# Optimization experiments

Measured on AMD Instinct MI355X. Metric: run time of the kernel, lower is better.

## Reference

```python
import jax, jax.numpy as jnp
import numpy as np

NUM_LAYERS = 3
CODEBOOK_SIZE = 2048
EMBED_DIM = 256
B, T = 16, 2048


def setup_inputs() -> dict:
    key = jax.random.key(0)
    k1, k2 = jax.random.split(key)
    h = jax.random.normal(k1, (B, T, EMBED_DIM), dtype=jnp.float32)
    codebooks = jax.random.normal(k2, (NUM_LAYERS, CODEBOOK_SIZE, EMBED_DIM), dtype=jnp.float32)
    return {"h": h, "codebooks": codebooks}


def reference(h, codebooks):
    """Residual VQ: 3 sequential layers of nearest-codeword quantization.
    h: (B, T, D); codebooks: (L, K, D).
    Returns (quantized_total (B,T,D), indices (L, B, T)).
    """
    residual = h
    quantized_total = jnp.zeros_like(h)
    all_indices = []
    for l in range(codebooks.shape[0]):
        W = codebooks[l]  # (K, D)
        # ||r - w||^2 = ||r||^2 - 2 r.w + ||w||^2 ; same argmin as the naive broadcast form.
        r_sq = jnp.sum(residual * residual, axis=-1, keepdims=True)         # (B, T, 1)
        w_sq = jnp.sum(W * W, axis=-1)                                      # (K,)
        cross = jnp.einsum('btd,kd->btk', residual, W)                      # (B, T, K)
        dists = r_sq - 2.0 * cross + w_sq                                   # (B, T, K)
        indices = jnp.argmin(dists, axis=-1)                                # (B, T)
        all_indices.append(indices)
        quant = W[indices]                                                  # gather -> (B, T, D)
        quantized_total = quantized_total + quant
        residual = residual - quant
    return quantized_total, jnp.stack(all_indices, axis=0)
```

## Files before the change

kernel.cpp:

```cpp
#include <hip/hip_runtime.h>
#include <math.h>

#define NUM_LAYERS 3
#define KCB 2048
#define DIM 256
#define NROWS 32768
#define NQ (NROWS * DIM)

#define F_BYTES (3u * 128u * 16384u)

#define BSH_OFF  0
#define XCH_OFF  65536
#define RSQP_OFF 98304
#define BV_OFF   99328
#define BI_OFF   100352
#define BIDX_OFF 101376
#define SMEM_BYTES 101888

typedef _Float16 half8 __attribute__((ext_vector_type(8)));
typedef float   f32x4 __attribute__((ext_vector_type(4)));

__global__ void rvq_wsq(const float* __restrict__ cb, float* __restrict__ wsq)
{
    int tid = blockIdx.x * 256 + threadIdx.x;
    const float* p = cb + (size_t)tid * DIM;
    float s = 0.f;
    #pragma unroll
    for (int u = 0; u < 64; ++u) {
        float4 v = *(const float4*)(p + u * 4);
        s = fmaf(v.x, v.x, s); s = fmaf(v.y, v.y, s);
        s = fmaf(v.z, v.z, s); s = fmaf(v.w, v.w, s);
    }
    wsq[tid] = s;
}

__global__ void rvq_repack(const float* __restrict__ cb, unsigned short* __restrict__ F)
{
    int b = blockIdx.x;
    int layer = b >> 10;
    int rem   = b & 1023;
    int tn    = rem >> 3;
    int kb    = rem & 7;
    int lane  = threadIdx.x;

    int cw = tn * 16 + (lane & 15);
    int k0 = kb * 32 + (lane >> 4) * 8;
    const float* src = cb + ((size_t)(layer * KCB + cw)) * DIM + k0;
    float4 x0 = *(const float4*)(src);
    float4 x1 = *(const float4*)(src + 4);
    float v[8] = {x0.x, x0.y, x0.z, x0.w, x1.x, x1.y, x1.z, x1.w};

    half8 hi, lo;
    #pragma unroll
    for (int j = 0; j < 8; ++j) {
        _Float16 h = (_Float16)v[j];
        hi[j] = h;
        lo[j] = (_Float16)(v[j] - (float)h);
    }
    size_t base = ((size_t)b) * 1024;
    *(half8*)(F + base + lane * 8)        = hi;
    *(half8*)(F + base + 512 + lane * 8)  = lo;
}

__device__ __forceinline__ void stage_chunk32(const char* Fb, char* dst, int c, int t)
{
    const char* g = Fb + (size_t)c * 32768;
    #pragma unroll
    for (int i = 0; i < 4; ++i) {
        int off = (i * 512 + t) * 16;
        __builtin_amdgcn_global_load_lds(
            (const __attribute__((address_space(1))) unsigned int*)(g + off),
            (__attribute__((address_space(3))) unsigned int*)(dst + off), 16, 0, 0);
    }
}

__device__ __forceinline__ void tile_partial(
    const char* tbase, const half8 (&ahi)[2][4], const half8 (&alo)[2][4],
    int kt, int lane, f32x4 (&po)[2])
{
    const f32x4 z = {0.f, 0.f, 0.f, 0.f};
    f32x4 a00 = z, a01 = z, a10 = z, a11 = z;
    #pragma unroll
    for (int kq = 0; kq < 4; ++kq) {
        const int kb = kt * 4 + kq;
        half8 bhi = *(const half8*)(tbase + kb * 2048 + lane * 16);
        half8 blo = *(const half8*)(tbase + kb * 2048 + 1024 + lane * 16);
        if (kq & 1) {
            a01 = __builtin_amdgcn_mfma_f32_16x16x32_f16(ahi[0][kq], bhi, a01, 0, 0, 0);
            a11 = __builtin_amdgcn_mfma_f32_16x16x32_f16(ahi[1][kq], bhi, a11, 0, 0, 0);
            a01 = __builtin_amdgcn_mfma_f32_16x16x32_f16(alo[0][kq], bhi, a01, 0, 0, 0);
            a11 = __builtin_amdgcn_mfma_f32_16x16x32_f16(alo[1][kq], bhi, a11, 0, 0, 0);
            a01 = __builtin_amdgcn_mfma_f32_16x16x32_f16(ahi[0][kq], blo, a01, 0, 0, 0);
            a11 = __builtin_amdgcn_mfma_f32_16x16x32_f16(ahi[1][kq], blo, a11, 0, 0, 0);
        } else {
            a00 = __builtin_amdgcn_mfma_f32_16x16x32_f16(ahi[0][kq], bhi, a00, 0, 0, 0);
            a10 = __builtin_amdgcn_mfma_f32_16x16x32_f16(ahi[1][kq], bhi, a10, 0, 0, 0);
            a00 = __builtin_amdgcn_mfma_f32_16x16x32_f16(alo[0][kq], bhi, a00, 0, 0, 0);
            a10 = __builtin_amdgcn_mfma_f32_16x16x32_f16(alo[1][kq], bhi, a10, 0, 0, 0);
            a00 = __builtin_amdgcn_mfma_f32_16x16x32_f16(ahi[0][kq], blo, a00, 0, 0, 0);
            a10 = __builtin_amdgcn_mfma_f32_16x16x32_f16(ahi[1][kq], blo, a10, 0, 0, 0);
        }
    }
    #pragma unroll
    for (int i = 0; i < 4; ++i) { po[0][i] = a00[i] + a01[i]; po[1][i] = a10[i] + a11[i]; }
}

__global__ __launch_bounds__(512, 2)
void rvq_main(const float* __restrict__ h,
              const float* __restrict__ cb,
              const unsigned short* __restrict__ F,
              const float* __restrict__ wsq,
              float* __restrict__ out)
{
    extern __shared__ char smem[];
    char*  Bsh     = smem + BSH_OFF;
    char*  Xch     = smem + XCH_OFF;
    float* rsqp    = (float*)(smem + RSQP_OFF);
    float* bV_sh   = (float*)(smem + BV_OFF);
    int*   bI_sh   = (int*)  (smem + BI_OFF);
    int*   bidx_sh = (int*)  (smem + BIDX_OFF);

    const int t     = threadIdx.x;
    const int lane  = t & 63;
    const int wv    = t >> 6;
    const int kt    = wv & 1;
    const int rg    = wv >> 1;
    const int rowB  = blockIdx.x * 128;
    const int row0w = rowB + rg * 32;
    const int arow  = lane & 15;
    const int aq    = lane >> 4;

    half8 ahi[2][4], alo[2][4];
    float s2[2];
    #pragma unroll
    for (int mi = 0; mi < 2; ++mi) {
        s2[mi] = 0.f;
        #pragma unroll
        for (int kq = 0; kq < 4; ++kq) {
            const float* p = h + (size_t)(row0w + mi * 16 + arow) * DIM + (kt * 4 + kq) * 32 + aq * 8;
            float4 x0 = *(const float4*)(p);
            float4 x1 = *(const float4*)(p + 4);
            float v[8] = {x0.x, x0.y, x0.z, x0.w, x1.x, x1.y, x1.z, x1.w};
            #pragma unroll
            for (int j = 0; j < 8; ++j) {
                _Float16 hv = (_Float16)v[j];
                ahi[mi][kq][j] = hv;
                alo[mi][kq][j] = (_Float16)(v[j] - (float)hv);
                s2[mi] = fmaf(v[j], v[j], s2[mi]);
            }
        }
    }

    stage_chunk32((const char*)F, Bsh, 0, t);

    for (int l = 0; l < NUM_LAYERS; ++l) {
        const float* __restrict__ Wl  = cb + (size_t)l * KCB * DIM;
        const float* __restrict__ wql = wsq + l * KCB;
        const char*  Fb = (const char*)F + (size_t)l * 2097152;

        float a0 = s2[0], a1 = s2[1];
        a0 += __shfl_xor(a0, 16); a0 += __shfl_xor(a0, 32);
        a1 += __shfl_xor(a1, 16); a1 += __shfl_xor(a1, 32);
        if (aq == 0) {
            rsqp[kt * 128 + rg * 32 + arow]      = a0;
            rsqp[kt * 128 + rg * 32 + 16 + arow] = a1;
        }
        __syncthreads();

        float rsqC[2][4];
        #pragma unroll
        for (int mi = 0; mi < 2; ++mi)
            #pragma unroll
            for (int i = 0; i < 4; ++i) {
                int row = rg * 32 + mi * 16 + aq * 4 + i;
                rsqC[mi][i] = rsqp[row] + rsqp[128 + row];
            }

        float bestV[2][4];
        int   bestI[2][4];
        #pragma unroll
        for (int mi = 0; mi < 2; ++mi)
            #pragma unroll
            for (int i = 0; i < 4; ++i) { bestV[mi][i] = INFINITY; bestI[mi][i] = 0; }

        for (int c = 0; c < 64; ++c) {
            const int cur = c & 1;
            if (c + 1 < 64) stage_chunk32(Fb, Bsh + (size_t)(1 - cur) * 32768, c + 1, t);
            const char* bb = Bsh + (size_t)cur * 32768;

            {
                f32x4 pn[2];
                tile_partial(bb + (size_t)(1 - kt) * 16384, ahi, alo, kt, lane, pn);
                char* xw = Xch + (size_t)cur * 16384 + rg * 4096 + kt * 2048;
                *(f32x4*)(xw + lane * 16)        = pn[0];
                *(f32x4*)(xw + 1024 + lane * 16) = pn[1];
            }
            f32x4 po[2];
            tile_partial(bb + (size_t)kt * 16384, ahi, alo, kt, lane, po);

            __syncthreads();

            const char* xr = Xch + (size_t)cur * 16384 + rg * 4096 + (1 - kt) * 2048;
            f32x4 pp0 = *(const f32x4*)(xr + lane * 16);
            f32x4 pp1 = *(const f32x4*)(xr + 1024 + lane * 16);

            const int col = c * 32 + kt * 16 + arow;
            const float wq = wql[col];
            #pragma unroll
            for (int i = 0; i < 4; ++i) {
                float c0 = po[0][i] + pp0[i];
                float d0 = (rsqC[0][i] - 2.f * c0) + wq;
                if (d0 < bestV[0][i]) { bestV[0][i] = d0; bestI[0][i] = col; }
                float c1 = po[1][i] + pp1[i];
                float d1 = (rsqC[1][i] - 2.f * c1) + wq;
                if (d1 < bestV[1][i]) { bestV[1][i] = d1; bestI[1][i] = col; }
            }
        }

        #pragma unroll
        for (int mi = 0; mi < 2; ++mi)
            #pragma unroll
            for (int i = 0; i < 4; ++i) {
                float bv = bestV[mi][i]; int bi = bestI[mi][i];
                #pragma unroll
                for (int s = 8; s; s >>= 1) {
                    float ov = __shfl_xor(bv, s, 16);
                    int   oi = __shfl_xor(bi, s, 16);
                    if (ov < bv || (ov == bv && oi < bi)) { bv = ov; bi = oi; }
                }
                bestV[mi][i] = bv; bestI[mi][i] = bi;
            }
        if (arow == 0) {
            #pragma unroll
            for (int mi = 0; mi < 2; ++mi)
                #pragma unroll
                for (int i = 0; i < 4; ++i) {
                    bV_sh[wv * 32 + mi * 16 + aq * 4 + i] = bestV[mi][i];
                    bI_sh[wv * 32 + mi * 16 + aq * 4 + i] = bestI[mi][i];
                }
        }
        __syncthreads();

        if (t < 128) {
            int rgi = t >> 5, rl = t & 31;
            float v0 = bV_sh[(rgi * 2 + 0) * 32 + rl]; int i0 = bI_sh[(rgi * 2 + 0) * 32 + rl];
            float v1 = bV_sh[(rgi * 2 + 1) * 32 + rl]; int i1 = bI_sh[(rgi * 2 + 1) * 32 + rl];
            int bi = (v1 < v0 || (v1 == v0 && i1 < i0)) ? i1 : i0;
            bidx_sh[t] = bi;
            out[NQ + (size_t)l * NROWS + rowB + t] = (float)bi;
        }
        if (l < NUM_LAYERS - 1)
            stage_chunk32(Fb + 2097152, Bsh, 0, t);
        __syncthreads();

        if (l < NUM_LAYERS - 1) {
            #pragma unroll
            for (int mi = 0; mi < 2; ++mi) {
                const int bi = bidx_sh[rg * 32 + mi * 16 + arow];
                const float* wrow = Wl + (size_t)bi * DIM;
                float ns = 0.f;
                #pragma unroll
                for (int kq = 0; kq < 4; ++kq) {
                    const float* wp = wrow + (kt * 4 + kq) * 32 + aq * 8;
                    float4 w0 = *(const float4*)(wp);
                    float4 w1 = *(const float4*)(wp + 4);
                    float wv8[8] = {w0.x, w0.y, w0.z, w0.w, w1.x, w1.y, w1.z, w1.w};
                    #pragma unroll
                    for (int j = 0; j < 8; ++j) {
                        float r = ((float)ahi[mi][kq][j] + (float)alo[mi][kq][j]) - wv8[j];
                        _Float16 hv = (_Float16)r;
                        ahi[mi][kq][j] = hv;
                        alo[mi][kq][j] = (_Float16)(r - (float)hv);
                        ns = fmaf(r, r, ns);
                    }
                }
                s2[mi] = ns;
            }
        } else {
            #pragma unroll
            for (int mi = 0; mi < 2; ++mi) {
                const int row = row0w + mi * 16 + arow;
                const int bi  = bidx_sh[rg * 32 + mi * 16 + arow];
                const float* wrow = Wl + (size_t)bi * DIM;
                #pragma unroll
                for (int kq = 0; kq < 4; ++kq) {
                    const int ko = (kt * 4 + kq) * 32 + aq * 8;
                    const float* wp = wrow + ko;
                    const float* hp = h + (size_t)row * DIM + ko;
                    float4 w0 = *(const float4*)(wp);
                    float4 w1 = *(const float4*)(wp + 4);
                    float4 h0 = *(const float4*)(hp);
                    float4 h1 = *(const float4*)(hp + 4);
                    float wv8[8] = {w0.x, w0.y, w0.z, w0.w, w1.x, w1.y, w1.z, w1.w};
                    float hv8[8] = {h0.x, h0.y, h0.z, h0.w, h1.x, h1.y, h1.z, h1.w};
                    float o[8];
                    #pragma unroll
                    for (int j = 0; j < 8; ++j) {
                        float r = ((float)ahi[mi][kq][j] + (float)alo[mi][kq][j]) - wv8[j];
                        o[j] = hv8[j] - r;
                    }
                    float* op = out + (size_t)row * DIM + ko;
                    *(float4*)(op)     = make_float4(o[0], o[1], o[2], o[3]);
                    *(float4*)(op + 4) = make_float4(o[4], o[5], o[6], o[7]);
                }
            }
        }
    }
}

extern "C" void kernel_launch(void* const* d_in, const int* in_sizes, int n_in,
                              void* d_out, int out_size, void* d_ws, size_t ws_size,
                              hipStream_t stream) {
    const float* h  = (const float*)d_in[0];
    const float* cb = (const float*)d_in[1];
    float* out = (float*)d_out;
    unsigned short* F = (unsigned short*)d_ws;
    float* wsq = (float*)((char*)d_ws + F_BYTES);

    hipFuncSetAttribute((const void*)rvq_main,
                        hipFuncAttributeMaxDynamicSharedMemorySize, SMEM_BYTES);

    rvq_wsq   <<<dim3(24),   dim3(256), 0, stream>>>(cb, wsq);
    rvq_repack<<<dim3(3072), dim3(64),  0, stream>>>(cb, F);
    rvq_main  <<<dim3(NROWS / 128), dim3(512), SMEM_BYTES, stream>>>(h, cb, F, wsq, out);
}
```

Baseline: 382.7 us.

## Give each wave full-K residual fragments and drop cross-wave partial-sum exchange

```diff
diff --git a/kernel.cpp b/kernel.cpp
--- a/kernel.cpp
+++ b/kernel.cpp
@@ -10,12 +10,11 @@
 #define F_BYTES (3u * 128u * 16384u)
 
 #define BSH_OFF  0
-#define XCH_OFF  65536
-#define RSQP_OFF 98304
-#define BV_OFF   99328
-#define BI_OFF   100352
-#define BIDX_OFF 101376
-#define SMEM_BYTES 101888
+#define BV_OFF   65536
+#define BI_OFF   66048
+#define BIDX_OFF 66560
+#define RSQ_OFF  66816
+#define SMEM_BYTES 67072
 
 typedef _Float16 half8 __attribute__((ext_vector_type(8)));
 typedef float   f32x4 __attribute__((ext_vector_type(4)));
@@ -66,46 +65,52 @@
 {
     const char* g = Fb + (size_t)c * 32768;
     #pragma unroll
-    for (int i = 0; i < 4; ++i) {
-        int off = (i * 512 + t) * 16;
+    for (int i = 0; i < 8; ++i) {
+        int off = (i * 256 + t) * 16;
         __builtin_amdgcn_global_load_lds(
             (const __attribute__((address_space(1))) unsigned int*)(g + off),
             (__attribute__((address_space(3))) unsigned int*)(dst + off), 16, 0, 0);
     }
 }
 
-__device__ __forceinline__ void tile_partial(
-    const char* tbase, const half8 (&ahi)[2][4], const half8 (&alo)[2][4],
-    int kt, int lane, f32x4 (&po)[2])
+__device__ __forceinline__ void tile_full(
+    const char* tbase, const half8 (&ahi)[2][8], const half8 (&alo)[2][8],
+    int lane, f32x4 (&po)[2])
 {
     const f32x4 z = {0.f, 0.f, 0.f, 0.f};
     f32x4 a00 = z, a01 = z, a10 = z, a11 = z;
-    #pragma unroll
-    for (int kq = 0; kq < 4; ++kq) {
-        const int kb = kt * 4 + kq;
-        half8 bhi = *(const half8*)(tbase + kb * 2048 + lane * 16);
-        half8 blo = *(const half8*)(tbase + kb * 2048 + 1024 + lane * 16);
-        if (kq & 1) {
-            a01 = __builtin_amdgcn_mfma_f32_16x16x32_f16(ahi[0][kq], bhi, a01, 0, 0, 0);
-            a11 = __builtin_amdgcn_mfma_f32_16x16x32_f16(ahi[1][kq], bhi, a11, 0, 0, 0);
-            a01 = __builtin_amdgcn_mfma_f32_16x16x32_f16(alo[0][kq], bhi, a01, 0, 0, 0);
-            a11 = __builtin_amdgcn_mfma_f32_16x16x32_f16(alo[1][kq], bhi, a11, 0, 0, 0);
-            a01 = __builtin_amdgcn_mfma_f32_16x16x32_f16(ahi[0][kq], blo, a01, 0, 0, 0);
-            a11 = __builtin_amdgcn_mfma_f32_16x16x32_f16(ahi[1][kq], blo, a11, 0, 0, 0);
+    const char* p = tbase + lane * 16;
+    half8 bhi = *(const half8*)(p);
+    half8 blo = *(const half8*)(p + 1024);
+    #pragma unroll
+    for (int kb = 0; kb < 8; ++kb) {
+        half8 nhi, nlo;
+        if (kb < 7) {
+            nhi = *(const half8*)(p + (kb + 1) * 2048);
+            nlo = *(const half8*)(p + (kb + 1) * 2048 + 1024);
+        }
+        if (kb & 1) {
+            a01 = __builtin_amdgcn_mfma_f32_16x16x32_f16(ahi[0][kb], bhi, a01, 0, 0, 0);
+            a11 = __builtin_amdgcn_mfma_f32_16x16x32_f16(ahi[1][kb], bhi, a11, 0, 0, 0);
+            a00 = __builtin_amdgcn_mfma_f32_16x16x32_f16(alo[0][kb], bhi, a00, 0, 0, 0);
+            a10 = __builtin_amdgcn_mfma_f32_16x16x32_f16(alo[1][kb], bhi, a10, 0, 0, 0);
+            a01 = __builtin_amdgcn_mfma_f32_16x16x32_f16(ahi[0][kb], blo, a01, 0, 0, 0);
+            a11 = __builtin_amdgcn_mfma_f32_16x16x32_f16(ahi[1][kb], blo, a11, 0, 0, 0);
         } else {
-            a00 = __builtin_amdgcn_mfma_f32_16x16x32_f16(ahi[0][kq], bhi, a00, 0, 0, 0);
-            a10 = __builtin_amdgcn_mfma_f32_16x16x32_f16(ahi[1][kq], bhi, a10, 0, 0, 0);
-            a00 = __builtin_amdgcn_mfma_f32_16x16x32_f16(alo[0][kq], bhi, a00, 0, 0, 0);
-            a10 = __builtin_amdgcn_mfma_f32_16x16x32_f16(alo[1][kq], bhi, a10, 0, 0, 0);
-            a00 = __builtin_amdgcn_mfma_f32_16x16x32_f16(ahi[0][kq], blo, a00, 0, 0, 0);
-            a10 = __builtin_amdgcn_mfma_f32_16x16x32_f16(ahi[1][kq], blo, a10, 0, 0, 0);
-        }
+            a00 = __builtin_amdgcn_mfma_f32_16x16x32_f16(ahi[0][kb], bhi, a00, 0, 0, 0);
+            a10 = __builtin_amdgcn_mfma_f32_16x16x32_f16(ahi[1][kb], bhi, a10, 0, 0, 0);
+            a01 = __builtin_amdgcn_mfma_f32_16x16x32_f16(alo[0][kb], bhi, a01, 0, 0, 0);
+            a11 = __builtin_amdgcn_mfma_f32_16x16x32_f16(alo[1][kb], bhi, a11, 0, 0, 0);
+            a00 = __builtin_amdgcn_mfma_f32_16x16x32_f16(ahi[0][kb], blo, a00, 0, 0, 0);
+            a10 = __builtin_amdgcn_mfma_f32_16x16x32_f16(ahi[1][kb], blo, a10, 0, 0, 0);
+        }
+        if (kb < 7) { bhi = nhi; blo = nlo; }
     }
     #pragma unroll
     for (int i = 0; i < 4; ++i) { po[0][i] = a00[i] + a01[i]; po[1][i] = a10[i] + a11[i]; }
 }
 
-__global__ __launch_bounds__(512, 2)
+__global__ __launch_bounds__(256, 2)
 void rvq_main(const float* __restrict__ h,
               const float* __restrict__ cb,
               const unsigned short* __restrict__ F,
@@ -114,38 +119,37 @@
 {
     extern __shared__ char smem[];
     char*  Bsh     = smem + BSH_OFF;
-    char*  Xch     = smem + XCH_OFF;
-    float* rsqp    = (float*)(smem + RSQP_OFF);
     float* bV_sh   = (float*)(smem + BV_OFF);
     int*   bI_sh   = (int*)  (smem + BI_OFF);
     int*   bidx_sh = (int*)  (smem + BIDX_OFF);
+    float* rsq_sh  = (float*)(smem + RSQ_OFF);
 
     const int t     = threadIdx.x;
     const int lane  = t & 63;
     const int wv    = t >> 6;
-    const int kt    = wv & 1;
+    const int ct    = wv & 1;
     const int rg    = wv >> 1;
-    const int rowB  = blockIdx.x * 128;
+    const int rowB  = blockIdx.x * 64;
     const int row0w = rowB + rg * 32;
     const int arow  = lane & 15;
     const int aq    = lane >> 4;
 
-    half8 ahi[2][4], alo[2][4];
+    half8 ahi[2][8], alo[2][8];
     float s2[2];
     #pragma unroll
     for (int mi = 0; mi < 2; ++mi) {
         s2[mi] = 0.f;
         #pragma unroll
-        for (int kq = 0; kq < 4; ++kq) {
-            const float* p = h + (size_t)(row0w + mi * 16 + arow) * DIM + (kt * 4 + kq) * 32 + aq * 8;
+        for (int kb = 0; kb < 8; ++kb) {
+            const float* p = h + (size_t)(row0w + mi * 16 + arow) * DIM + kb * 32 + aq * 8;
             float4 x0 = *(const float4*)(p);
             float4 x1 = *(const float4*)(p + 4);
             float v[8] = {x0.x, x0.y, x0.z, x0.w, x1.x, x1.y, x1.z, x1.w};
             #pragma unroll
             for (int j = 0; j < 8; ++j) {
                 _Float16 hv = (_Float16)v[j];
-                ahi[mi][kq][j] = hv;
-                alo[mi][kq][j] = (_Float16)(v[j] - (float)hv);
+                ahi[mi][kb][j] = hv;
+                alo[mi][kb][j] = (_Float16)(v[j] - (float)hv);
                 s2[mi] = fmaf(v[j], v[j], s2[mi]);
             }
         }
@@ -161,9 +165,9 @@
         float a0 = s2[0], a1 = s2[1];
         a0 += __shfl_xor(a0, 16); a0 += __shfl_xor(a0, 32);
         a1 += __shfl_xor(a1, 16); a1 += __shfl_xor(a1, 32);
-        if (aq == 0) {
-            rsqp[kt * 128 + rg * 32 + arow]      = a0;
-            rsqp[kt * 128 + rg * 32 + 16 + arow] = a1;
+        if (aq == 0 && ct == 0) {
+            rsq_sh[rg * 32 + arow]      = a0;
+            rsq_sh[rg * 32 + 16 + arow] = a1;
         }
         __syncthreads();
 
@@ -171,10 +175,8 @@
         #pragma unroll
         for (int mi = 0; mi < 2; ++mi)
             #pragma unroll
-            for (int i = 0; i < 4; ++i) {
-                int row = rg * 32 + mi * 16 + aq * 4 + i;
-                rsqC[mi][i] = rsqp[row] + rsqp[128 + row];
-            }
+            for (int i = 0; i < 4; ++i)
+                rsqC[mi][i] = rsq_sh[rg * 32 + mi * 16 + aq * 4 + i];
 
         float bestV[2][4];
         int   bestI[2][4];
@@ -186,35 +188,20 @@
         for (int c = 0; c < 64; ++c) {
             const int cur = c & 1;
             if (c + 1 < 64) stage_chunk32(Fb, Bsh + (size_t)(1 - cur) * 32768, c + 1, t);
-            const char* bb = Bsh + (size_t)cur * 32768;
-
-            {
-                f32x4 pn[2];
-                tile_partial(bb + (size_t)(1 - kt) * 16384, ahi, alo, kt, lane, pn);
-                char* xw = Xch + (size_t)cur * 16384 + rg * 4096 + kt * 2048;
-                *(f32x4*)(xw + lane * 16)        = pn[0];
-                *(f32x4*)(xw + 1024 + lane * 16) = pn[1];
-            }
+
             f32x4 po[2];
-            tile_partial(bb + (size_t)kt * 16384, ahi, alo, kt, lane, po);
-
+            tile_full(Bsh + (size_t)cur * 32768 + (size_t)ct * 16384, ahi, alo, lane, po);
+
+            const int col = c * 32 + ct * 16 + arow;
+            const float wq = wql[col];
+            #pragma unroll
+            for (int i = 0; i < 4; ++i) {
+                float d0 = (rsqC[0][i] - 2.f * po[0][i]) + wq;
+                if (d0 < bestV[0][i]) { bestV[0][i] = d0; bestI[0][i] = col; }
+                float d1 = (rsqC[1][i] - 2.f * po[1][i]) + wq;
+                if (d1 < bestV[1][i]) { bestV[1][i] = d1; bestI[1][i] = col; }
+            }
             __syncthreads();
-
-            const char* xr = Xch + (size_t)cur * 16384 + rg * 4096 + (1 - kt) * 2048;
-            f32x4 pp0 = *(const f32x4*)(xr + lane * 16);
-            f32x4 pp1 = *(const f32x4*)(xr + 1024 + lane * 16);
-
-            const int col = c * 32 + kt * 16 + arow;
-            const float wq = wql[col];
-            #pragma unroll
-            for (int i = 0; i < 4; ++i) {
-                float c0 = po[0][i] + pp0[i];
-                float d0 = (rsqC[0][i] - 2.f * c0) + wq;
-                if (d0 < bestV[0][i]) { bestV[0][i] = d0; bestI[0][i] = col; }
-                float c1 = po[1][i] + pp1[i];
-                float d1 = (rsqC[1][i] - 2.f * c1) + wq;
-                if (d1 < bestV[1][i]) { bestV[1][i] = d1; bestI[1][i] = col; }
-            }
         }
 
         #pragma unroll
@@ -241,7 +228,7 @@
         }
         __syncthreads();
 
-        if (t < 128) {
+        if (t < 64) {
             int rgi = t >> 5, rl = t & 31;
             float v0 = bV_sh[(rgi * 2 + 0) * 32 + rl]; int i0 = bI_sh[(rgi * 2 + 0) * 32 + rl];
             float v1 = bV_sh[(rgi * 2 + 1) * 32 + rl]; int i1 = bI_sh[(rgi * 2 + 1) * 32 + rl];
@@ -260,17 +247,17 @@
                 const float* wrow = Wl + (size_t)bi * DIM;
                 float ns = 0.f;
                 #pragma unroll
-                for (int kq = 0; kq < 4; ++kq) {
-                    const float* wp = wrow + (kt * 4 + kq) * 32 + aq * 8;
+                for (int kb = 0; kb < 8; ++kb) {
+                    const float* wp = wrow + kb * 32 + aq * 8;
                     float4 w0 = *(const float4*)(wp);
                     float4 w1 = *(const float4*)(wp + 4);
                     float wv8[8] = {w0.x, w0.y, w0.z, w0.w, w1.x, w1.y, w1.z, w1.w};
                     #pragma unroll
                     for (int j = 0; j < 8; ++j) {
-                        float r = ((float)ahi[mi][kq][j] + (float)alo[mi][kq][j]) - wv8[j];
+                        float r = ((float)ahi[mi][kb][j] + (float)alo[mi][kb][j]) - wv8[j];
                         _Float16 hv = (_Float16)r;
-                        ahi[mi][kq][j] = hv;
-                        alo[mi][kq][j] = (_Float16)(r - (float)hv);
+                        ahi[mi][kb][j] = hv;
+                        alo[mi][kb][j] = (_Float16)(r - (float)hv);
                         ns = fmaf(r, r, ns);
                     }
                 }
@@ -284,7 +271,8 @@
                 const float* wrow = Wl + (size_t)bi * DIM;
                 #pragma unroll
                 for (int kq = 0; kq < 4; ++kq) {
-                    const int ko = (kt * 4 + kq) * 32 + aq * 8;
+                    const int kb = ct * 4 + kq;
+                    const int ko = kb * 32 + aq * 8;
                     const float* wp = wrow + ko;
                     const float* hp = h + (size_t)row * DIM + ko;
                     float4 w0 = *(const float4*)(wp);
@@ -296,7 +284,7 @@
                     float o[8];
                     #pragma unroll
                     for (int j = 0; j < 8; ++j) {
-                        float r = ((float)ahi[mi][kq][j] + (float)alo[mi][kq][j]) - wv8[j];
+                        float r = ((float)ahi[mi][kb][j] + (float)alo[mi][kb][j]) - wv8[j];
                         o[j] = hv8[j] - r;
                     }
                     float* op = out + (size_t)row * DIM + ko;
@@ -322,5 +310,5 @@
 
     rvq_wsq   <<<dim3(24),   dim3(256), 0, stream>>>(cb, wsq);
     rvq_repack<<<dim3(3072), dim3(64),  0, stream>>>(cb, F);
-    rvq_main  <<<dim3(NROWS / 128), dim3(512), SMEM_BYTES, stream>>>(h, cb, F, wsq, out);
-}
+    rvq_main  <<<dim3(NROWS / 64), dim3(256), SMEM_BYTES, stream>>>(h, cb, F, wsq, out);
+}
```

Result: slower. 415.7 us (+8.6%).

## Software-pipeline distance epilogue behind next chunk's MFMAs and prefetch B fragments

Applied to the files above, without the earlier changes.

```diff
diff --git a/kernel.cpp b/kernel.cpp
--- a/kernel.cpp
+++ b/kernel.cpp
@@ -74,17 +74,23 @@
     }
 }
 
-__device__ __forceinline__ void tile_partial(
+__device__ __forceinline__ void tile_partial_pl(
     const char* tbase, const half8 (&ahi)[2][4], const half8 (&alo)[2][4],
     int kt, int lane, f32x4 (&po)[2])
 {
     const f32x4 z = {0.f, 0.f, 0.f, 0.f};
     f32x4 a00 = z, a01 = z, a10 = z, a11 = z;
+    const char* p = tbase + kt * 4 * 2048 + lane * 16;
+    half8 bhi = *(const half8*)(p);
+    half8 blo = *(const half8*)(p + 1024);
     #pragma unroll
     for (int kq = 0; kq < 4; ++kq) {
-        const int kb = kt * 4 + kq;
-        half8 bhi = *(const half8*)(tbase + kb * 2048 + lane * 16);
-        half8 blo = *(const half8*)(tbase + kb * 2048 + 1024 + lane * 16);
+        half8 nhi, nlo;
+        if (kq < 3) {
+            nhi = *(const half8*)(p + (kq + 1) * 2048);
+            nlo = *(const half8*)(p + (kq + 1) * 2048 + 1024);
+            __builtin_amdgcn_sched_group_barrier(0x100, 2, 0);
+        }
         if (kq & 1) {
             a01 = __builtin_amdgcn_mfma_f32_16x16x32_f16(ahi[0][kq], bhi, a01, 0, 0, 0);
             a11 = __builtin_amdgcn_mfma_f32_16x16x32_f16(ahi[1][kq], bhi, a11, 0, 0, 0);
@@ -100,6 +106,8 @@
             a00 = __builtin_amdgcn_mfma_f32_16x16x32_f16(ahi[0][kq], blo, a00, 0, 0, 0);
             a10 = __builtin_amdgcn_mfma_f32_16x16x32_f16(ahi[1][kq], blo, a10, 0, 0, 0);
         }
+        __builtin_amdgcn_sched_group_barrier(0x8, 6, 0);
+        if (kq < 3) { bhi = nhi; blo = nlo; }
     }
     #pragma unroll
     for (int i = 0; i < 4; ++i) { po[0][i] = a00[i] + a01[i]; po[1][i] = a10[i] + a11[i]; }
@@ -183,35 +191,81 @@
             #pragma unroll
             for (int i = 0; i < 4; ++i) { bestV[mi][i] = INFINITY; bestI[mi][i] = 0; }
 
-        for (int c = 0; c < 64; ++c) {
+        f32x4 po_prev[2];
+
+        {
+            stage_chunk32(Fb, Bsh + 32768, 1, t);
+            const char* bb = Bsh;
+            __builtin_amdgcn_s_setprio(1);
+            {
+                f32x4 pn[2];
+                tile_partial_pl(bb + (size_t)(1 - kt) * 16384, ahi, alo, kt, lane, pn);
+                char* xw = Xch + rg * 4096 + kt * 2048;
+                *(f32x4*)(xw + lane * 16)        = pn[0];
+                *(f32x4*)(xw + 1024 + lane * 16) = pn[1];
+            }
+            tile_partial_pl(bb + (size_t)kt * 16384, ahi, alo, kt, lane, po_prev);
+            __builtin_amdgcn_s_setprio(0);
+            asm volatile("s_waitcnt vmcnt(0) lgkmcnt(0)" ::: "memory");
+            __builtin_amdgcn_sched_barrier(0);
+            __builtin_amdgcn_s_barrier();
+        }
+
+        for (int c = 1; c < 64; ++c) {
             const int cur = c & 1;
             if (c + 1 < 64) stage_chunk32(Fb, Bsh + (size_t)(1 - cur) * 32768, c + 1, t);
             const char* bb = Bsh + (size_t)cur * 32768;
 
+            const char* xr = Xch + (size_t)(1 - cur) * 16384 + rg * 4096 + (1 - kt) * 2048;
+            f32x4 pp0 = *(const f32x4*)(xr + lane * 16);
+            f32x4 pp1 = *(const f32x4*)(xr + 1024 + lane * 16);
+
+            __builtin_amdgcn_s_setprio(1);
+            f32x4 pn[2];
+            tile_partial_pl(bb + (size_t)(1 - kt) * 16384, ahi, alo, kt, lane, pn);
+            __builtin_amdgcn_s_setprio(0);
+
             {
-                f32x4 pn[2];
-                tile_partial(bb + (size_t)(1 - kt) * 16384, ahi, alo, kt, lane, pn);
+                const int col = (c - 1) * 32 + kt * 16 + arow;
+                const float wq = wql[col];
+                #pragma unroll
+                for (int i = 0; i < 4; ++i) {
+                    float c0 = po_prev[0][i] + pp0[i];
+                    float d0 = (rsqC[0][i] - 2.f * c0) + wq;
+                    if (d0 < bestV[0][i]) { bestV[0][i] = d0; bestI[0][i] = col; }
+                    float c1 = po_prev[1][i] + pp1[i];
+                    float d1 = (rsqC[1][i] - 2.f * c1) + wq;
+                    if (d1 < bestV[1][i]) { bestV[1][i] = d1; bestI[1][i] = col; }
+                }
+            }
+
+            {
                 char* xw = Xch + (size_t)cur * 16384 + rg * 4096 + kt * 2048;
                 *(f32x4*)(xw + lane * 16)        = pn[0];
                 *(f32x4*)(xw + 1024 + lane * 16) = pn[1];
             }
-            f32x4 po[2];
-            tile_partial(bb + (size_t)kt * 16384, ahi, alo, kt, lane, po);
-
-            __syncthreads();
-
-            const char* xr = Xch + (size_t)cur * 16384 + rg * 4096 + (1 - kt) * 2048;
+
+            __builtin_amdgcn_s_setprio(1);
+            tile_partial_pl(bb + (size_t)kt * 16384, ahi, alo, kt, lane, po_prev);
+            __builtin_amdgcn_s_setprio(0);
+
+            asm volatile("s_waitcnt vmcnt(0) lgkmcnt(0)" ::: "memory");
+            __builtin_amdgcn_sched_barrier(0);
+            __builtin_amdgcn_s_barrier();
+        }
+
+        {
+            const char* xr = Xch + 16384 + rg * 4096 + (1 - kt) * 2048;
             f32x4 pp0 = *(const f32x4*)(xr + lane * 16);
             f32x4 pp1 = *(const f32x4*)(xr + 1024 + lane * 16);
-
-            const int col = c * 32 + kt * 16 + arow;
+            const int col = 63 * 32 + kt * 16 + arow;
             const float wq = wql[col];
             #pragma unroll
             for (int i = 0; i < 4; ++i) {
-                float c0 = po[0][i] + pp0[i];
+                float c0 = po_prev[0][i] + pp0[i];
                 float d0 = (rsqC[0][i] - 2.f * c0) + wq;
                 if (d0 < bestV[0][i]) { bestV[0][i] = d0; bestI[0][i] = col; }
-                float c1 = po[1][i] + pp1[i];
+                float c1 = po_prev[1][i] + pp1[i];
                 float d1 = (rsqC[1][i] - 2.f * c1) + wq;
                 if (d1 < bestV[1][i]) { bestV[1][i] = d1; bestI[1][i] = col; }
             }
```

Result: no change. 386.3 us (+0.9%).

## Load codebook fragments directly from global, drop LDS staging and row-norm term

Applied to the files above, without the earlier changes.

```diff
diff --git a/kernel.cpp b/kernel.cpp
--- a/kernel.cpp
+++ b/kernel.cpp
@@ -9,13 +9,11 @@
 
 #define F_BYTES (3u * 128u * 16384u)
 
-#define BSH_OFF  0
-#define XCH_OFF  65536
-#define RSQP_OFF 98304
-#define BV_OFF   99328
-#define BI_OFF   100352
-#define BIDX_OFF 101376
-#define SMEM_BYTES 101888
+#define XCH_OFF  0
+#define BV_OFF   32768
+#define BI_OFF   33792
+#define BIDX_OFF 34816
+#define SMEM_BYTES 35328
 
 typedef _Float16 half8 __attribute__((ext_vector_type(8)));
 typedef float   f32x4 __attribute__((ext_vector_type(4)));
@@ -62,43 +60,36 @@
     *(half8*)(F + base + 512 + lane * 8)  = lo;
 }
 
-__device__ __forceinline__ void stage_chunk32(const char* Fb, char* dst, int c, int t)
-{
-    const char* g = Fb + (size_t)c * 32768;
-    #pragma unroll
-    for (int i = 0; i < 4; ++i) {
-        int off = (i * 512 + t) * 16;
-        __builtin_amdgcn_global_load_lds(
-            (const __attribute__((address_space(1))) unsigned int*)(g + off),
-            (__attribute__((address_space(3))) unsigned int*)(dst + off), 16, 0, 0);
-    }
-}
-
-__device__ __forceinline__ void tile_partial(
-    const char* tbase, const half8 (&ahi)[2][4], const half8 (&alo)[2][4],
-    int kt, int lane, f32x4 (&po)[2])
+__device__ __forceinline__ void tile_direct(
+    const unsigned short* __restrict__ p,
+    const half8 (&ahi)[2][4], const half8 (&alo)[2][4],
+    f32x4 (&po)[2])
 {
     const f32x4 z = {0.f, 0.f, 0.f, 0.f};
     f32x4 a00 = z, a01 = z, a10 = z, a11 = z;
+    half8 bh[4], bl[4];
+    bh[0] = *(const half8*)(p);        bl[0] = *(const half8*)(p + 512);
+    bh[1] = *(const half8*)(p + 1024); bl[1] = *(const half8*)(p + 1536);
     #pragma unroll
     for (int kq = 0; kq < 4; ++kq) {
-        const int kb = kt * 4 + kq;
-        half8 bhi = *(const half8*)(tbase + kb * 2048 + lane * 16);
-        half8 blo = *(const half8*)(tbase + kb * 2048 + 1024 + lane * 16);
+        if (kq < 2) {
+            bh[kq + 2] = *(const half8*)(p + (kq + 2) * 1024);
+            bl[kq + 2] = *(const half8*)(p + (kq + 2) * 1024 + 512);
+        }
         if (kq & 1) {
-            a01 = __builtin_amdgcn_mfma_f32_16x16x32_f16(ahi[0][kq], bhi, a01, 0, 0, 0);
-            a11 = __builtin_amdgcn_mfma_f32_16x16x32_f16(ahi[1][kq], bhi, a11, 0, 0, 0);
-            a01 = __builtin_amdgcn_mfma_f32_16x16x32_f16(alo[0][kq], bhi, a01, 0, 0, 0);
-            a11 = __builtin_amdgcn_mfma_f32_16x16x32_f16(alo[1][kq], bhi, a11, 0, 0, 0);
-            a01 = __builtin_amdgcn_mfma_f32_16x16x32_f16(ahi[0][kq], blo, a01, 0, 0, 0);
-            a11 = __builtin_amdgcn_mfma_f32_16x16x32_f16(ahi[1][kq], blo, a11, 0, 0, 0);
+            a01 = __builtin_amdgcn_mfma_f32_16x16x32_f16(ahi[0][kq], bh[kq], a01, 0, 0, 0);
+            a11 = __builtin_amdgcn_mfma_f32_16x16x32_f16(ahi[1][kq], bh[kq], a11, 0, 0, 0);
+            a01 = __builtin_amdgcn_mfma_f32_16x16x32_f16(alo[0][kq], bh[kq], a01, 0, 0, 0);
+            a11 = __builtin_amdgcn_mfma_f32_16x16x32_f16(alo[1][kq], bh[kq], a11, 0, 0, 0);
+            a01 = __builtin_amdgcn_mfma_f32_16x16x32_f16(ahi[0][kq], bl[kq], a01, 0, 0, 0);
+            a11 = __builtin_amdgcn_mfma_f32_16x16x32_f16(ahi[1][kq], bl[kq], a11, 0, 0, 0);
         } else {
-            a00 = __builtin_amdgcn_mfma_f32_16x16x32_f16(ahi[0][kq], bhi, a00, 0, 0, 0);
-            a10 = __builtin_amdgcn_mfma_f32_16x16x32_f16(ahi[1][kq], bhi, a10, 0, 0, 0);
-            a00 = __builtin_amdgcn_mfma_f32_16x16x32_f16(alo[0][kq], bhi, a00, 0, 0, 0);
-            a10 = __builtin_amdgcn_mfma_f32_16x16x32_f16(alo[1][kq], bhi, a10, 0, 0, 0);
-            a00 = __builtin_amdgcn_mfma_f32_16x16x32_f16(ahi[0][kq], blo, a00, 0, 0, 0);
-            a10 = __builtin_amdgcn_mfma_f32_16x16x32_f16(ahi[1][kq], blo, a10, 0, 0, 0);
+            a00 = __builtin_amdgcn_mfma_f32_16x16x32_f16(ahi[0][kq], bh[kq], a00, 0, 0, 0);
+            a10 = __builtin_amdgcn_mfma_f32_16x16x32_f16(ahi[1][kq], bh[kq], a10, 0, 0, 0);
+            a00 = __builtin_amdgcn_mfma_f32_16x16x32_f16(alo[0][kq], bh[kq], a00, 0, 0, 0);
+            a10 = __builtin_amdgcn_mfma_f32_16x16x32_f16(alo[1][kq], bh[kq], a10, 0, 0, 0);
+            a00 = __builtin_amdgcn_mfma_f32_16x16x32_f16(ahi[0][kq], bl[kq], a00, 0, 0, 0);
+            a10 = __builtin_amdgcn_mfma_f32_16x16x32_f16(ahi[1][kq], bl[kq], a10, 0, 0, 0);
         }
     }
     #pragma unroll
@@ -113,9 +104,7 @@
               float* __restrict__ out)
 {
     extern __shared__ char smem[];
-    char*  Bsh     = smem + BSH_OFF;
     char*  Xch     = smem + XCH_OFF;
-    float* rsqp    = (float*)(smem + RSQP_OFF);
     float* bV_sh   = (float*)(smem + BV_OFF);
     int*   bI_sh   = (int*)  (smem + BI_OFF);
     int*   bidx_sh = (int*)  (smem + BIDX_OFF);
@@ -131,10 +120,8 @@
     const int aq    = lane >> 4;
 
     half8 ahi[2][4], alo[2][4];
-    float s2[2];
     #pragma unroll
     for (int mi = 0; mi < 2; ++mi) {
-        s2[mi] = 0.f;
         #pragma unroll
         for (int kq = 0; kq < 4; ++kq) {
             const float* p = h + (size_t)(row0w + mi * 16 + arow) * DIM + (kt * 4 + kq) * 32 + aq * 8;
@@ -146,35 +133,14 @@
                 _Float16 hv = (_Float16)v[j];
                 ahi[mi][kq][j] = hv;
                 alo[mi][kq][j] = (_Float16)(v[j] - (float)hv);
-                s2[mi] = fmaf(v[j], v[j], s2[mi]);
-            }
-        }
-    }
-
-    stage_chunk32((const char*)F, Bsh, 0, t);
+            }
+        }
+    }
 
     for (int l = 0; l < NUM_LAYERS; ++l) {
         const float* __restrict__ Wl  = cb + (size_t)l * KCB * DIM;
         const float* __restrict__ wql = wsq + l * KCB;
-        const char*  Fb = (const char*)F + (size_t)l * 2097152;
-
-        float a0 = s2[0], a1 = s2[1];
-        a0 += __shfl_xor(a0, 16); a0 += __shfl_xor(a0, 32);
-        a1 += __shfl_xor(a1, 16); a1 += __shfl_xor(a1, 32);
-        if (aq == 0) {
-            rsqp[kt * 128 + rg * 32 + arow]      = a0;
-            rsqp[kt * 128 + rg * 32 + 16 + arow] = a1;
-        }
-        __syncthreads();
-
-        float rsqC[2][4];
-        #pragma unroll
-        for (int mi = 0; mi < 2; ++mi)
-            #pragma unroll
-            for (int i = 0; i < 4; ++i) {
-                int row = rg * 32 + mi * 16 + aq * 4 + i;
-                rsqC[mi][i] = rsqp[row] + rsqp[128 + row];
-            }
+        const unsigned short* Fl = F + (size_t)l * 1048576 + kt * 4096 + lane * 8;
 
         float bestV[2][4];
         int   bestI[2][4];
@@ -183,38 +149,41 @@
             #pragma unroll
             for (int i = 0; i < 4; ++i) { bestV[mi][i] = INFINITY; bestI[mi][i] = 0; }
 
+        float wq_cur = wql[kt * 16 + arow];
+
         for (int c = 0; c < 64; ++c) {
             const int cur = c & 1;
-            if (c + 1 < 64) stage_chunk32(Fb, Bsh + (size_t)(1 - cur) * 32768, c + 1, t);
-            const char* bb = Bsh + (size_t)cur * 32768;
+            float wq_next = (c < 63) ? wql[(c + 1) * 32 + kt * 16 + arow] : 0.f;
+            const unsigned short* Ftile = Fl + (size_t)c * 16384;
 
             {
                 f32x4 pn[2];
-                tile_partial(bb + (size_t)(1 - kt) * 16384, ahi, alo, kt, lane, pn);
+                tile_direct(Ftile + (size_t)(1 - kt) * 8192, ahi, alo, pn);
                 char* xw = Xch + (size_t)cur * 16384 + rg * 4096 + kt * 2048;
                 *(f32x4*)(xw + lane * 16)        = pn[0];
                 *(f32x4*)(xw + 1024 + lane * 16) = pn[1];
             }
             f32x4 po[2];
-            tile_partial(bb + (size_t)kt * 16384, ahi, alo, kt, lane, po);
-
-            __syncthreads();
+            tile_direct(Ftile + (size_t)kt * 8192, ahi, alo, po);
+
+            asm volatile("s_waitcnt lgkmcnt(0)" ::: "memory");
+            __builtin_amdgcn_sched_barrier(0);
+            __builtin_amdgcn_s_barrier();
+            __builtin_amdgcn_sched_barrier(0);
 
             const char* xr = Xch + (size_t)cur * 16384 + rg * 4096 + (1 - kt) * 2048;
             f32x4 pp0 = *(const f32x4*)(xr + lane * 16);
             f32x4 pp1 = *(const f32x4*)(xr + 1024 + lane * 16);
 
             const int col = c * 32 + kt * 16 + arow;
-            const float wq = wql[col];
             #pragma unroll
             for (int i = 0; i < 4; ++i) {
-                float c0 = po[0][i] + pp0[i];
-                float d0 = (rsqC[0][i] - 2.f * c0) + wq;
+                float d0 = fmaf(-2.f, po[0][i] + pp0[i], wq_cur);
                 if (d0 < bestV[0][i]) { bestV[0][i] = d0; bestI[0][i] = col; }
-                float c1 = po[1][i] + pp1[i];
-                float d1 = (rsqC[1][i] - 2.f * c1) + wq;
+                float d1 = fmaf(-2.f, po[1][i] + pp1[i], wq_cur);
                 if (d1 < bestV[1][i]) { bestV[1][i] = d1; bestI[1][i] = col; }
             }
+            wq_cur = wq_next;
         }
 
         #pragma unroll
@@ -249,8 +218,6 @@
             bidx_sh[t] = bi;
             out[NQ + (size_t)l * NROWS + rowB + t] = (float)bi;
         }
-        if (l < NUM_LAYERS - 1)
-            stage_chunk32(Fb + 2097152, Bsh, 0, t);
         __syncthreads();
 
         if (l < NUM_LAYERS - 1) {
@@ -258,7 +225,6 @@
             for (int mi = 0; mi < 2; ++mi) {
                 const int bi = bidx_sh[rg * 32 + mi * 16 + arow];
                 const float* wrow = Wl + (size_t)bi * DIM;
-                float ns = 0.f;
                 #pragma unroll
                 for (int kq = 0; kq < 4; ++kq) {
                     const float* wp = wrow + (kt * 4 + kq) * 32 + aq * 8;
@@ -271,10 +237,8 @@
                         _Float16 hv = (_Float16)r;
                         ahi[mi][kq][j] = hv;
                         alo[mi][kq][j] = (_Float16)(r - (float)hv);
-                        ns = fmaf(r, r, ns);
                     }
                 }
-                s2[mi] = ns;
             }
         } else {
             #pragma unroll
```

Measured after the change: 468.5 us. 1.22x slower.
